# Kernel tuning notes

Measured on AMD Instinct MI355X. Metric: run time of the kernel, lower is better.

Reference implementation:

```python
import jax, jax.numpy as jnp
import numpy as np

B, S, D, H, L = 512, 128, 128, 1024, 128
N_SUB = 4  # fixed dopri5 substeps per observation interval

# Dormand-Prince 5(4) tableau (FSAL form); solution uses 5th-order b weights.
DP_A = (
    (),
    (1/5,),
    (3/40, 9/40),
    (44/45, -56/15, 32/9),
    (19372/6561, -25360/2187, 64448/6561, -212/729),
    (9017/3168, -355/33, 46732/5247, 49/176, -5103/18656),
    (35/384, 0.0, 500/1113, 125/192, -2187/6784, 11/84),
)
DP_B = (35/384, 0.0, 500/1113, 125/192, -2187/6784, 11/84, 0.0)


def _mlp(h, w0, b0, w1, b1, w2, b2):
    # create_mlp(hidden, hidden, hidden, num_layers=3, 'tanh'): Lin-tanh-Lin-tanh-Lin
    h = jnp.tanh(h @ w0.T + b0)
    h = jnp.tanh(h @ w1.T + b1)
    return h @ w2.T + b2


def _gru_cell(x, h, w_ih, w_hh, b_ih, b_hh):
    gi = x @ w_ih.T + b_ih  # [B, 3H]
    gh = h @ w_hh.T + b_hh
    i_r, i_z, i_n = jnp.split(gi, 3, axis=-1)
    h_r, h_z, h_n = jnp.split(gh, 3, axis=-1)
    r = jax.nn.sigmoid(i_r + h_r)
    z = jax.nn.sigmoid(i_z + h_z)
    n = jnp.tanh(i_n + r * h_n)
    return (1.0 - z) * n + z * h


def _dopri5_step(f, h, hs):
    ks = []
    for row in DP_A:
        y = h
        for a, k in zip(row, ks):
            if a != 0.0:
                y = y + (hs * a) * k
        ks.append(f(y))
    out = h
    for b, k in zip(DP_B, ks):
        if b != 0.0:
            out = out + (hs * b) * k
    return out


def _forward(x, t, gru_w_ih, gru_w_hh, gru_b_ih, gru_b_hh,
             w0, b0, w1, b1, w2, b2, mu_w, mu_b, lv_w, lv_b):
    f = lambda h: _mlp(h, w0, b0, w1, b1, w2, b2)  # autonomous ODE func
    bsz = x.shape[0]
    hdim = gru_w_hh.shape[1]
    dts = t[0, 1:, 0] - t[0, :-1, 0]  # [S-1]
    h = _gru_cell(x[:, 0, :], jnp.zeros((bsz, hdim), x.dtype),
                  gru_w_ih, gru_w_hh, gru_b_ih, gru_b_hh)

    def step(h, inp):
        xi, dt = inp
        hs = dt / N_SUB
        for _ in range(N_SUB):
            h = _dopri5_step(f, h, hs)
        h = _gru_cell(xi, h, gru_w_ih, gru_w_hh, gru_b_ih, gru_b_hh)
        return h, None

    h, _ = jax.lax.scan(step, h, (jnp.swapaxes(x[:, 1:, :], 0, 1), dts))
    mu = h @ mu_w.T + mu_b
    logvar = h @ lv_w.T + lv_b
    return mu, logvar


def setup_inputs() -> dict:
    key = jax.random.key(0)
    ks = jax.random.split(key, 12)
    s = 0.02
    return {
        "x": jax.random.normal(ks[0], (B, S, D), jnp.float32),
        "t": jnp.arange(S, dtype=jnp.float32).reshape(1, S, 1) * 0.1,
        "gru_w_ih": jax.random.normal(ks[1], (3 * H, D), jnp.float32) * s,
        "gru_w_hh": jax.random.normal(ks[2], (3 * H, H), jnp.float32) * s,
        "gru_b_ih": jnp.zeros((3 * H,), jnp.float32),
        "gru_b_hh": jnp.zeros((3 * H,), jnp.float32),
        "w0": jax.random.normal(ks[3], (H, H), jnp.float32) * s,
        "b0": jnp.zeros((H,), jnp.float32),
        "w1": jax.random.normal(ks[4], (H, H), jnp.float32) * s,
        "b1": jnp.zeros((H,), jnp.float32),
        "w2": jax.random.normal(ks[5], (H, H), jnp.float32) * s,
        "b2": jnp.zeros((H,), jnp.float32),
        "mu_w": jax.random.normal(ks[6], (L, H), jnp.float32) * s,
        "mu_b": jnp.zeros((L,), jnp.float32),
        "lv_w": jax.random.normal(ks[7], (L, H), jnp.float32) * s,
        "lv_b": jnp.zeros((L,), jnp.float32),
    }


def reference(x, t, gru_w_ih, gru_w_hh, gru_b_ih, gru_b_hh,
              w0, b0, w1, b1, w2, b2, mu_w, mu_b, lv_w, lv_b):
    return _forward(x, t, gru_w_ih, gru_w_hh, gru_b_ih, gru_b_hh,
                    w0, b0, w1, b1, w2, b2, mu_w, mu_b, lv_w, lv_b)
```

## Files before the change

kernel.cpp:

```cpp
#include <hip/hip_runtime.h>
#include <hip/hip_cooperative_groups.h>
#include <math.h>

#define Bz 512
#define Sz 128
#define Dz 128
#define Hz 1024
#define Lz 128
#define NSUB 4

#define GRID 256
#define BLOCK 512
#define NGRP 16
#define GBLK 16

typedef _Float16 half8 __attribute__((ext_vector_type(8)));
typedef float floatx4 __attribute__((ext_vector_type(4)));
typedef unsigned long long u64;

#define MFMA16(a, b, c) __builtin_amdgcn_mfma_f32_16x16x32_f16(a, b, c, 0, 0, 0)

#define ALO_D 4096
#define BHI_O 8192
#define BLO_D 8192
#define CHUNK_HALFS 24576
#define LDS_HALFS 49152

enum { EPI_F32 = 0, EPI_T = 1, EPI_Y = 2, EPI_H = 3 };

__constant__ float DPA_C[6][6] = {
  {0.2f, 0.f, 0.f, 0.f, 0.f, 0.f},
  {0.075f, 0.225f, 0.f, 0.f, 0.f, 0.f},
  {44.f/45.f, -56.f/15.f, 32.f/9.f, 0.f, 0.f, 0.f},
  {19372.f/6561.f, -25360.f/2187.f, 64448.f/6561.f, -212.f/729.f, 0.f, 0.f},
  {9017.f/3168.f, -355.f/33.f, 46732.f/5247.f, 49.f/176.f, -5103.f/18656.f, 0.f},
  {35.f/384.f, 0.f, 500.f/1113.f, 125.f/192.f, -2187.f/6784.f, 11.f/84.f},
};

struct KArgs {
  const float *x, *t, *w_ih, *w_hh, *b_ih, *b_hh;
  const float *w0, *b0, *w1, *b1, *w2, *b2, *mu_w, *mu_b, *lv_w, *lv_b;
  float* out;
  float *h, *gi, *gh;
  unsigned* bar;
  _Float16 *yh, *yl, *t1h, *t1l, *t2h, *t2l, *hhp, *hlp;
  _Float16 *w0h, *w0l, *w1h, *w1l, *w2h, *w2l;
  _Float16 *whhh, *whhl, *wihh, *wihl, *muh, *mulo, *lvh, *lvl;
};

__device__ __forceinline__ float ldc1(const float* p) {
  unsigned v = __hip_atomic_load((unsigned*)p, __ATOMIC_RELAXED, __HIP_MEMORY_SCOPE_AGENT);
  union { unsigned u; float f; } c; c.u = v; return c.f;
}
__device__ __forceinline__ void stc1(float* p, float f) {
  union { float f; unsigned u; } c; c.f = f;
  __hip_atomic_store((unsigned*)p, c.u, __ATOMIC_RELAXED, __HIP_MEMORY_SCOPE_AGENT);
}
__device__ __forceinline__ half8 ldc8h(const _Float16* p) {
  union { u64 u[2]; half8 h; } c;
  c.u[0] = __hip_atomic_load((const u64*)p, __ATOMIC_RELAXED, __HIP_MEMORY_SCOPE_AGENT);
  c.u[1] = __hip_atomic_load(((const u64*)p) + 1, __ATOMIC_RELAXED, __HIP_MEMORY_SCOPE_AGENT);
  return c.h;
}
__device__ __forceinline__ void sth2(_Float16* ph, _Float16* pl, float v) {
  _Float16 h = (_Float16)v;
  _Float16 l = (_Float16)((v - (float)h) * 2048.0f);
  union { _Float16 f; unsigned short u; } ch, cl; ch.f = h; cl.f = l;
  __hip_atomic_store((unsigned short*)ph, ch.u, __ATOMIC_RELAXED, __HIP_MEMORY_SCOPE_AGENT);
  __hip_atomic_store((unsigned short*)pl, cl.u, __ATOMIC_RELAXED, __HIP_MEMORY_SCOPE_AGENT);
}

__device__ __forceinline__ void gbar(unsigned* gb, int jj, unsigned e) {
  asm volatile("s_waitcnt vmcnt(0) lgkmcnt(0)" ::: "memory");
  __syncthreads();
  if (threadIdx.x == 0)
    __hip_atomic_store(&gb[jj], e, __ATOMIC_RELAXED, __HIP_MEMORY_SCOPE_AGENT);
  if (threadIdx.x < 64) {
    const int sl = threadIdx.x & 15;
    while (__hip_atomic_load(&gb[sl], __ATOMIC_RELAXED, __HIP_MEMORY_SCOPE_AGENT) != e)
      __builtin_amdgcn_s_sleep(1);
  }
  __syncthreads();
}

__device__ __forceinline__ void split8(float4 a, float4 b, half8& h, half8& l) {
  float v[8] = {a.x, a.y, a.z, a.w, b.x, b.y, b.z, b.w};
#pragma unroll
  for (int i = 0; i < 8; ++i) {
    _Float16 hh = (_Float16)v[i];
    h[i] = hh;
    l[i] = (_Float16)((v[i] - (float)hh) * 2048.0f);
  }
}

__device__ void convW(const float* __restrict__ W, size_t total,
                      _Float16* __restrict__ hi, _Float16* __restrict__ lo) {
  for (size_t i = (size_t)blockIdx.x * BLOCK + threadIdx.x; i < total;
       i += (size_t)GRID * BLOCK) {
    const float v = W[i];
    const _Float16 h = (_Float16)v;
    hi[i] = h;
    lo[i] = (_Float16)((v - (float)h) * 2048.0f);
  }
}

template<int K, int AM>
__device__ __forceinline__ void mfma_tile(
    const float* __restrict__ Af,
    const _Float16* __restrict__ Ahi, const _Float16* __restrict__ Alo, int lda,
    const _Float16* __restrict__ Whi, const _Float16* __restrict__ Wlo,
    const float* __restrict__ bias,
    float* __restrict__ Cf, _Float16* __restrict__ Chi, _Float16* __restrict__ Clo,
    int ldc, int act, int epi, int stage, float hs,
    const float* __restrict__ hbuf,
    floatx4& K0, floatx4& K1, floatx4& K2, floatx4& K3, floatx4& K4,
    floatx4& Hc,
    int row0, int col0, _Float16* __restrict__ lds)
{
  constexpr int NC = K >> 7;
  const int tid = threadIdx.x;
  const int ln  = tid & 63;
  const int l16 = ln & 15;
  const int qd  = ln >> 4;
  const int wv  = tid >> 6;
  const int wr  = wv >> 2;
  const int wc  = wv & 3;

  const int an   = tid >> 4;
  const int an15 = an & 15, ang = an >> 4;
  const int seg  = tid & 15;
  const int c_ = seg >> 2, q_ = seg & 3;
  const int ua = q_ * 16 + (an15 ^ ((q_ << 1) | (c_ & 1)));
  const int aoff  = (((c_ * 2 + ang) * 64 + ua) << 3);
  const int boff0 = BHI_O + (((c_ * 4 + ang) * 64 + ua) << 3);
  const int boff1 = BHI_O + (((c_ * 4 + 2 + ang) * 64 + ua) << 3);

  const float*    gA  = Af  + (size_t)(row0 + an) * lda + (seg << 3);
  const _Float16* gAh = Ahi + (size_t)(row0 + an) * lda + (seg << 3);
  const _Float16* gAl = Alo + (size_t)(row0 + an) * lda + (seg << 3);
  const _Float16* gW0h = Whi + (size_t)(col0 + an) * K + (seg << 3);
  const _Float16* gW0l = Wlo + (size_t)(col0 + an) * K + (seg << 3);
  const _Float16* gW1h = Whi + (size_t)(col0 + 32 + an) * K + (seg << 3);
  const _Float16* gW1l = Wlo + (size_t)(col0 + 32 + an) * K + (seg << 3);

  floatx4 Phh = {0,0,0,0}, Phl = {0,0,0,0}, Plh = {0,0,0,0}, Pll = {0,0,0,0};

  half8 rah, ral, rw0h, rw0l, rw1h, rw1l;
  float4 ra0, ra1;
  auto load6 = [&](int kk) {
    if (AM == 0) {
      rah = ldc8h(gAh + kk);
      ral = ldc8h(gAl + kk);
    } else {
      ra0 = *(const float4*)(gA + kk);
      ra1 = *(const float4*)(gA + kk + 4);
    }
    rw0h = *(const half8*)(gW0h + kk); rw0l = *(const half8*)(gW0l + kk);
    rw1h = *(const half8*)(gW1h + kk); rw1l = *(const half8*)(gW1l + kk);
  };
  auto store6 = [&](int bufo) {
    if (AM == 1) { half8 h, l; split8(ra0, ra1, h, l); rah = h; ral = l; }
    *(half8*)&lds[bufo + aoff]  = rah;
    *(half8*)&lds[bufo + aoff + ALO_D]  = ral;
    *(half8*)&lds[bufo + boff0] = rw0h;
    *(half8*)&lds[bufo + boff0 + BLO_D] = rw0l;
    *(half8*)&lds[bufo + boff1] = rw1h;
    *(half8*)&lds[bufo + boff1 + BLO_D] = rw1l;
  };

  load6(0);
  __syncthreads();
  store6(0);
  if (NC > 1) load6(128);

#pragma unroll
  for (int c = 0; c < NC; ++c) {
    __syncthreads();
    if (c + 1 < NC) {
      store6(((c + 1) & 1) ? CHUNK_HALFS : 0);
      if (c + 2 < NC) load6((c + 2) << 7);
    }
    const _Float16* __restrict__ lr = lds + ((c & 1) ? CHUNK_HALFS : 0);
#pragma unroll
    for (int kq = 0; kq < 4; ++kq) {
      const int lnw = ln ^ ((qd << 1) | (kq & 1));
      const int ab = ((kq * 2 + wr) * 64 + lnw) << 3;
      const int bb = BHI_O + (((kq * 4 + wc) * 64 + lnw) << 3);
      half8 ah = *(const half8*)&lr[ab];
      half8 al = *(const half8*)&lr[ab + ALO_D];
      half8 bh = *(const half8*)&lr[bb];
      half8 bl = *(const half8*)&lr[bb + BLO_D];
      Phh = MFMA16(ah, bh, Phh);
      Phl = MFMA16(ah, bl, Phl);
      Plh = MFMA16(al, bh, Plh);
      Pll = MFMA16(al, bl, Pll);
    }
  }

  const int col   = col0 + (wc << 4) + l16;
  const int rbase = row0 + (wr << 4) + (qd << 2);
  const float bb = bias[col];
#pragma unroll
  for (int i = 0; i < 4; ++i) {
    float v = Phh[i] + (Phl[i] + Plh[i]) * (1.0f/2048.0f)
            + Pll[i] * (1.0f/4194304.0f) + bb;
    if (act) v = tanhf(v);
    const size_t off = (size_t)(rbase + i) * ldc + col;
    if (epi == EPI_F32) {
      stc1(&Cf[off], v);
    } else if (epi == EPI_T) {
      sth2(Chi + off, Clo + off, v);
    } else {
      if (stage == 0) Hc[i] = ldc1(&hbuf[off]);
      float yv = Hc[i];
      const float* DP = DPA_C[stage];
      if (stage > 0) yv = fmaf(hs * DP[0], K0[i], yv);
      if (stage > 1) { float c1 = DP[1]; if (c1 != 0.f) yv = fmaf(hs * c1, K1[i], yv); }
      if (stage > 2) yv = fmaf(hs * DP[2], K2[i], yv);
      if (stage > 3) yv = fmaf(hs * DP[3], K3[i], yv);
      if (stage > 4) yv = fmaf(hs * DP[4], K4[i], yv);
      yv = fmaf(hs * DP[stage], v, yv);
      if      (stage == 0) K0[i] = v;
      else if (stage == 1) K1[i] = v;
      else if (stage == 2) K2[i] = v;
      else if (stage == 3) K3[i] = v;
      else if (stage == 4) K4[i] = v;
      if (epi == EPI_H) stc1(&Cf[off], yv);
      sth2(Chi + off, Clo + off, yv);
    }
  }
}

template<int K, int AM>
__device__ __forceinline__ void run_phase(
    const float* Af, const _Float16* Ahi, const _Float16* Alo, int lda,
    const _Float16* Whi, const _Float16* Wlo, const float* bias, int N,
    float* Cf, _Float16* Chi, _Float16* Clo, int ldc,
    int act, int epi, int stage, float hs, const float* hbuf,
    floatx4& K0, floatx4& K1, floatx4& K2, floatx4& K3, floatx4& K4,
    floatx4& Hc, int g, int jj, _Float16* lds)
{
  const int tilesN = N >> 6;
  const int row0 = g << 5;
  if (tilesN >= GBLK) {
    const int tn0 = ((jj & 7) << 1) | (jj >> 3);
    for (int i = 0; i < (tilesN >> 4); ++i)
      mfma_tile<K, AM>(Af, Ahi, Alo, lda, Whi, Wlo, bias, Cf, Chi, Clo, ldc,
                       act, epi, stage, hs, hbuf, K0, K1, K2, K3, K4, Hc,
                       row0, (tn0 + (i << 4)) << 6, lds);
  } else {
    if (jj < tilesN)
      mfma_tile<K, AM>(Af, Ahi, Alo, lda, Whi, Wlo, bias, Cf, Chi, Clo, ldc,
                       act, epi, stage, hs, hbuf, K0, K1, K2, K3, K4, Hc,
                       row0, jj << 6, lds);
  }
}

__global__ __launch_bounds__(BLOCK, 2) void ode_gru_kernel(KArgs a) {
  __shared__ __align__(16) _Float16 lds[LDS_HALFS];
  const int g  = blockIdx.x >> 4;
  const int jj = blockIdx.x & 15;
  unsigned* gb = a.bar + (g << 6);
  unsigned ep = 0;

  for (int i = jj * BLOCK + threadIdx.x; i < 32 * Hz; i += GBLK * BLOCK) {
    const size_t o = (size_t)g * 32 * Hz + i;
    stc1(a.h + o, 0.f);
    sth2(a.hhp + o, a.hlp + o, 0.f);
  }

  const size_t E1 = (size_t)Hz * Hz, Ehh = 3 * E1;
  const size_t Eih = (size_t)3 * Hz * Dz, Emu = (size_t)Lz * Hz;
  convW(a.w0,   E1,  a.w0h,  a.w0l);
  convW(a.w1,   E1,  a.w1h,  a.w1l);
  convW(a.w2,   E1,  a.w2h,  a.w2l);
  convW(a.w_hh, Ehh, a.whhh, a.whhl);
  convW(a.w_ih, Eih, a.wihh, a.wihl);
  convW(a.mu_w, Emu, a.muh,  a.mulo);
  convW(a.lv_w, Emu, a.lvh,  a.lvl);
  cooperative_groups::this_grid().sync();

  floatx4 K0 = {0,0,0,0}, K1 = {0,0,0,0}, K2 = {0,0,0,0};
  floatx4 K3 = {0,0,0,0}, K4 = {0,0,0,0}, Hc = {0,0,0,0};

  for (int s = 0; s < Sz; ++s) {
    if (s > 0) {
      const float dt = a.t[s] - a.t[s - 1];
      const float hs = dt * (1.0f / NSUB);
      for (int sub = 0; sub < NSUB; ++sub) {
        for (int st = 0; st < 6; ++st) {
          const _Float16* ah = (st == 0) ? a.hhp : a.yh;
          const _Float16* al = (st == 0) ? a.hlp : a.yl;
          run_phase<Hz, 0>(nullptr, ah, al, Hz, a.w0h, a.w0l, a.b0, Hz,
                           nullptr, a.t1h, a.t1l, Hz, 1, EPI_T, 0, 0.f, nullptr,
                           K0, K1, K2, K3, K4, Hc, g, jj, lds);
          gbar(gb, jj, ++ep);
          run_phase<Hz, 0>(nullptr, a.t1h, a.t1l, Hz, a.w1h, a.w1l, a.b1, Hz,
                           nullptr, a.t2h, a.t2l, Hz, 1, EPI_T, 0, 0.f, nullptr,
                           K0, K1, K2, K3, K4, Hc, g, jj, lds);
          gbar(gb, jj, ++ep);
          if (st < 5) {
            run_phase<Hz, 0>(nullptr, a.t2h, a.t2l, Hz, a.w2h, a.w2l, a.b2, Hz,
                             nullptr, a.yh, a.yl, Hz, 0, EPI_Y, st, hs, a.h,
                             K0, K1, K2, K3, K4, Hc, g, jj, lds);
          } else {
            run_phase<Hz, 0>(nullptr, a.t2h, a.t2l, Hz, a.w2h, a.w2l, a.b2, Hz,
                             a.h, a.hhp, a.hlp, Hz, 0, EPI_H, 5, hs, a.h,
                             K0, K1, K2, K3, K4, Hc, g, jj, lds);
          }
          gbar(gb, jj, ++ep);
        }
      }
    }

    run_phase<Dz, 1>(a.x + (size_t)s * Dz, nullptr, nullptr, Sz * Dz,
                     a.wihh, a.wihl, a.b_ih, 3 * Hz,
                     a.gi, nullptr, nullptr, 3 * Hz, 0, EPI_F32, 0, 0.f, nullptr,
                     K0, K1, K2, K3, K4, Hc, g, jj, lds);
    run_phase<Hz, 0>(nullptr, a.hhp, a.hlp, Hz, a.whhh, a.whhl, a.b_hh, 3 * Hz,
                     a.gh, nullptr, nullptr, 3 * Hz, 0, EPI_F32, 0, 0.f, nullptr,
                     K0, K1, K2, K3, K4, Hc, g, jj, lds);
    gbar(gb, jj, ++ep);

    for (int i = jj * BLOCK + threadIdx.x; i < 32 * Hz; i += GBLK * BLOCK) {
      const int r = g * 32 + (i >> 10);
      const int c = i & (Hz - 1);
      const size_t gx = (size_t)r * 3 * Hz + c;
      const size_t hx = (size_t)r * Hz + c;
      const float ir  = ldc1(a.gi + gx);
      const float iz  = ldc1(a.gi + gx + Hz);
      const float inn = ldc1(a.gi + gx + 2 * Hz);
      const float hr  = ldc1(a.gh + gx);
      const float hzv = ldc1(a.gh + gx + Hz);
      const float hnn = ldc1(a.gh + gx + 2 * Hz);
      const float hv  = ldc1(a.h + hx);
      const float rr  = 1.f / (1.f + expf(-(ir + hr)));
      const float zz  = 1.f / (1.f + expf(-(iz + hzv)));
      const float nnv = tanhf(inn + rr * hnn);
      const float hn  = (1.f - zz) * nnv + zz * hv;
      stc1(a.h + hx, hn);
      sth2(a.hhp + hx, a.hlp + hx, hn);
    }
    gbar(gb, jj, ++ep);
  }

  run_phase<Hz, 0>(nullptr, a.hhp, a.hlp, Hz, a.muh, a.mulo, a.mu_b, Lz,
                   a.out, nullptr, nullptr, Lz, 0, EPI_F32, 0, 0.f, nullptr,
                   K0, K1, K2, K3, K4, Hc, g, jj, lds);
  run_phase<Hz, 0>(nullptr, a.hhp, a.hlp, Hz, a.lvh, a.lvl, a.lv_b, Lz,
                   a.out + (size_t)Bz * Lz, nullptr, nullptr, Lz,
                   0, EPI_F32, 0, 0.f, nullptr,
                   K0, K1, K2, K3, K4, Hc, g, jj, lds);
}

extern "C" void kernel_launch(void* const* d_in, const int* in_sizes, int n_in,
                              void* d_out, int out_size, void* d_ws, size_t ws_size,
                              hipStream_t stream) {
  KArgs a;
  a.x    = (const float*)d_in[0];
  a.t    = (const float*)d_in[1];
  a.w_ih = (const float*)d_in[2];
  a.w_hh = (const float*)d_in[3];
  a.b_ih = (const float*)d_in[4];
  a.b_hh = (const float*)d_in[5];
  a.w0   = (const float*)d_in[6];
  a.b0   = (const float*)d_in[7];
  a.w1   = (const float*)d_in[8];
  a.b1   = (const float*)d_in[9];
  a.w2   = (const float*)d_in[10];
  a.b2   = (const float*)d_in[11];
  a.mu_w = (const float*)d_in[12];
  a.mu_b = (const float*)d_in[13];
  a.lv_w = (const float*)d_in[14];
  a.lv_b = (const float*)d_in[15];
  a.out  = (float*)d_out;

  float* ws = (float*)d_ws;
  const size_t BH = (size_t)Bz * Hz;
  a.h  = ws;
  a.gi = ws + BH;
  a.gh = ws + 4 * BH;
  a.bar = (unsigned*)(ws + 7 * BH);

  _Float16* hv = (_Float16*)(ws + 7 * BH + 1024);
  a.yh  = hv; hv += BH;  a.yl  = hv; hv += BH;
  a.t1h = hv; hv += BH;  a.t1l = hv; hv += BH;
  a.t2h = hv; hv += BH;  a.t2l = hv; hv += BH;
  a.hhp = hv; hv += BH;  a.hlp = hv; hv += BH;
  const size_t E1 = (size_t)Hz * Hz, Ehh = 3 * E1;
  const size_t Eih = (size_t)3 * Hz * Dz, Emu = (size_t)Lz * Hz;
  a.w0h = hv; hv += E1;  a.w0l = hv; hv += E1;
  a.w1h = hv; hv += E1;  a.w1l = hv; hv += E1;
  a.w2h = hv; hv += E1;  a.w2l = hv; hv += E1;
  a.whhh = hv; hv += Ehh; a.whhl = hv; hv += Ehh;
  a.wihh = hv; hv += Eih; a.wihl = hv; hv += Eih;
  a.muh = hv; hv += Emu; a.mulo = hv; hv += Emu;
  a.lvh = hv; hv += Emu; a.lvl = hv; hv += Emu;
  (void)ws_size; (void)in_sizes; (void)n_in; (void)out_size;

  KArgs args_val = a;
  void* params[] = { &args_val };
  hipLaunchCooperativeKernel((void*)ode_gru_kernel, dim3(GRID), dim3(BLOCK),
                             params, 0, stream);
}
```

Baseline: 87.76 ms.

## Switch tile GEMM to 32x32 MFMA with split-K across waves and LDS reduction

New measurement: 126.3 ms. 1.44x slower.

```diff
diff --git a/kernel.cpp b/kernel.cpp
--- a/kernel.cpp
+++ b/kernel.cpp
@@ -16,15 +16,14 @@
 
 typedef _Float16 half8 __attribute__((ext_vector_type(8)));
 typedef float floatx4 __attribute__((ext_vector_type(4)));
+typedef float floatx16 __attribute__((ext_vector_type(16)));
 typedef unsigned long long u64;
 
-#define MFMA16(a, b, c) __builtin_amdgcn_mfma_f32_16x16x32_f16(a, b, c, 0, 0, 0)
-
-#define ALO_D 4096
-#define BHI_O 8192
-#define BLO_D 8192
+#define MFMA32(a, b, c) __builtin_amdgcn_mfma_f32_32x32x16_f16(a, b, c, 0, 0, 0)
+
 #define CHUNK_HALFS 24576
 #define LDS_HALFS 49152
+#define PR 36
 
 enum { EPI_F32 = 0, EPI_T = 1, EPI_Y = 2, EPI_H = 3 };
 
@@ -123,17 +122,18 @@
   const int l16 = ln & 15;
   const int qd  = ln >> 4;
   const int wv  = tid >> 6;
-  const int wr  = wv >> 2;
+  const int wr  = (wv >> 2) & 1;
   const int wc  = wv & 3;
-
-  const int an   = tid >> 4;
-  const int an15 = an & 15, ang = an >> 4;
-  const int seg  = tid & 15;
-  const int c_ = seg >> 2, q_ = seg & 3;
-  const int ua = q_ * 16 + (an15 ^ ((q_ << 1) | (c_ & 1)));
-  const int aoff  = (((c_ * 2 + ang) * 64 + ua) << 3);
-  const int boff0 = BHI_O + (((c_ * 4 + ang) * 64 + ua) << 3);
-  const int boff1 = BHI_O + (((c_ * 4 + 2 + ang) * 64 + ua) << 3);
+  const int pos = wv & 1;
+  const int ks  = wv >> 1;
+
+  const int an  = tid >> 4;
+  const int seg = tid & 15;
+  const int stw = seg >> 1, bw = seg & 1;
+  const int usw = (an + (bw << 5)) ^ (((stw & 3) << 1) | bw);
+  const int aoff  = (stw * 64 + usw) << 3;
+  const int boff0 = 8192 + aoff;
+  const int boff1 = 12288 + aoff;
 
   const float*    gA  = Af  + (size_t)(row0 + an) * lda + (seg << 3);
   const _Float16* gAh = Ahi + (size_t)(row0 + an) * lda + (seg << 3);
@@ -143,7 +143,10 @@
   const _Float16* gW1h = Whi + (size_t)(col0 + 32 + an) * K + (seg << 3);
   const _Float16* gW1l = Wlo + (size_t)(col0 + 32 + an) * K + (seg << 3);
 
-  floatx4 Phh = {0,0,0,0}, Phl = {0,0,0,0}, Plh = {0,0,0,0}, Pll = {0,0,0,0};
+  floatx16 Phh = {0,0,0,0,0,0,0,0,0,0,0,0,0,0,0,0};
+  floatx16 Phl = {0,0,0,0,0,0,0,0,0,0,0,0,0,0,0,0};
+  floatx16 Plh = {0,0,0,0,0,0,0,0,0,0,0,0,0,0,0,0};
+  floatx16 Pll = {0,0,0,0,0,0,0,0,0,0,0,0,0,0,0,0};
 
   half8 rah, ral, rw0h, rw0l, rw1h, rw1l;
   float4 ra0, ra1;
@@ -160,12 +163,12 @@
   };
   auto store6 = [&](int bufo) {
     if (AM == 1) { half8 h, l; split8(ra0, ra1, h, l); rah = h; ral = l; }
-    *(half8*)&lds[bufo + aoff]  = rah;
-    *(half8*)&lds[bufo + aoff + ALO_D]  = ral;
-    *(half8*)&lds[bufo + boff0] = rw0h;
-    *(half8*)&lds[bufo + boff0 + BLO_D] = rw0l;
-    *(half8*)&lds[bufo + boff1] = rw1h;
-    *(half8*)&lds[bufo + boff1 + BLO_D] = rw1l;
+    *(half8*)&lds[bufo + aoff]          = rah;
+    *(half8*)&lds[bufo + aoff + 4096]   = ral;
+    *(half8*)&lds[bufo + boff0]         = rw0h;
+    *(half8*)&lds[bufo + boff0 + 8192]  = rw0l;
+    *(half8*)&lds[bufo + boff1]         = rw1h;
+    *(half8*)&lds[bufo + boff1 + 8192]  = rw1l;
   };
 
   load6(0);
@@ -180,30 +183,58 @@
       store6(((c + 1) & 1) ? CHUNK_HALFS : 0);
       if (c + 2 < NC) load6((c + 2) << 7);
     }
-    const _Float16* __restrict__ lr = lds + ((c & 1) ? CHUNK_HALFS : 0);
+    if ((c & 3) == ks) {
+      const _Float16* __restrict__ lr = lds + ((c & 1) ? CHUNK_HALFS : 0);
 #pragma unroll
-    for (int kq = 0; kq < 4; ++kq) {
-      const int lnw = ln ^ ((qd << 1) | (kq & 1));
-      const int ab = ((kq * 2 + wr) * 64 + lnw) << 3;
-      const int bb = BHI_O + (((kq * 4 + wc) * 64 + lnw) << 3);
-      half8 ah = *(const half8*)&lr[ab];
-      half8 al = *(const half8*)&lr[ab + ALO_D];
-      half8 bh = *(const half8*)&lr[bb];
-      half8 bl = *(const half8*)&lr[bb + BLO_D];
-      Phh = MFMA16(ah, bh, Phh);
-      Phl = MFMA16(ah, bl, Phl);
-      Plh = MFMA16(al, bh, Plh);
-      Pll = MFMA16(al, bl, Pll);
-    }
-  }
+      for (int st = 0; st < 8; ++st) {
+        const int usr = ln ^ (((st & 3) << 1) | (ln >> 5));
+        const int o = (st * 64 + usr) << 3;
+        half8 ah = *(const half8*)&lr[o];
+        half8 al = *(const half8*)&lr[o + 4096];
+        half8 bh = *(const half8*)&lr[8192 + pos * 4096 + o];
+        half8 bl = *(const half8*)&lr[16384 + pos * 4096 + o];
+        Phh = MFMA32(ah, bh, Phh);
+        Phl = MFMA32(ah, bl, Phl);
+        Plh = MFMA32(al, bh, Plh);
+        Pll = MFMA32(al, bl, Pll);
+      }
+    }
+  }
+
+  __syncthreads();
+  float* pf = (float*)lds;
+  {
+    const int c32w = ln & 31, b5 = ln >> 5;
+#pragma unroll
+    for (int jg = 0; jg < 4; ++jg) {
+      const int rb = 8 * jg + 4 * b5;
+      float4 v;
+      v.x = Phh[jg*4+0] + (Phl[jg*4+0] + Plh[jg*4+0]) * (1.0f/2048.0f)
+          + Pll[jg*4+0] * (1.0f/4194304.0f);
+      v.y = Phh[jg*4+1] + (Phl[jg*4+1] + Plh[jg*4+1]) * (1.0f/2048.0f)
+          + Pll[jg*4+1] * (1.0f/4194304.0f);
+      v.z = Phh[jg*4+2] + (Phl[jg*4+2] + Plh[jg*4+2]) * (1.0f/2048.0f)
+          + Pll[jg*4+2] * (1.0f/4194304.0f);
+      v.w = Phh[jg*4+3] + (Phl[jg*4+3] + Plh[jg*4+3]) * (1.0f/2048.0f)
+          + Pll[jg*4+3] * (1.0f/4194304.0f);
+      *(float4*)&pf[(wv * 32 + c32w) * PR + rb] = v;
+    }
+  }
+  __syncthreads();
 
   const int col   = col0 + (wc << 4) + l16;
   const int rbase = row0 + (wr << 4) + (qd << 2);
+  const int pos_e = wc >> 1;
+  const int c32e  = ((wc & 1) << 4) + l16;
+  const int re    = (wr << 4) + (qd << 2);
+  floatx4 p0 = *(const floatx4*)&pf[((0 + pos_e) * 32 + c32e) * PR + re];
+  floatx4 p1 = *(const floatx4*)&pf[((2 + pos_e) * 32 + c32e) * PR + re];
+  floatx4 p2 = *(const floatx4*)&pf[((4 + pos_e) * 32 + c32e) * PR + re];
+  floatx4 p3 = *(const floatx4*)&pf[((6 + pos_e) * 32 + c32e) * PR + re];
   const float bb = bias[col];
 #pragma unroll
   for (int i = 0; i < 4; ++i) {
-    float v = Phh[i] + (Phl[i] + Plh[i]) * (1.0f/2048.0f)
-            + Pll[i] * (1.0f/4194304.0f) + bb;
+    float v = p0[i] + p1[i] + p2[i] + p3[i] + bb;
     if (act) v = tanhf(v);
     const size_t off = (size_t)(rbase + i) * ldc + col;
     if (epi == EPI_F32) {
```

## Split K chunks across wave halves with LDS cross-wave reduction in MFMA tile

Applied to the files above, without the earlier changes.

Result: slower. 108.6 ms (+23.8%).

```diff
diff --git a/kernel.cpp b/kernel.cpp
--- a/kernel.cpp
+++ b/kernel.cpp
@@ -123,8 +123,10 @@
   const int l16 = ln & 15;
   const int qd  = ln >> 4;
   const int wv  = tid >> 6;
-  const int wr  = wv >> 2;
+  const int wr  = (wv >> 2) & 1;
   const int wc  = wv & 3;
+  const int pos = wv & 3;
+  const int ks  = wv >> 2;
 
   const int an   = tid >> 4;
   const int an15 = an & 15, ang = an >> 4;
@@ -143,7 +145,11 @@
   const _Float16* gW1h = Whi + (size_t)(col0 + 32 + an) * K + (seg << 3);
   const _Float16* gW1l = Wlo + (size_t)(col0 + 32 + an) * K + (seg << 3);
 
-  floatx4 Phh = {0,0,0,0}, Phl = {0,0,0,0}, Plh = {0,0,0,0}, Pll = {0,0,0,0};
+  floatx4 acc[2][4];
+#pragma unroll
+  for (int f = 0; f < 2; ++f)
+#pragma unroll
+    for (int p = 0; p < 4; ++p) acc[f][p] = (floatx4){0, 0, 0, 0};
 
   half8 rah, ral, rw0h, rw0l, rw1h, rw1l;
   float4 ra0, ra1;
@@ -160,11 +166,11 @@
   };
   auto store6 = [&](int bufo) {
     if (AM == 1) { half8 h, l; split8(ra0, ra1, h, l); rah = h; ral = l; }
-    *(half8*)&lds[bufo + aoff]  = rah;
+    *(half8*)&lds[bufo + aoff]          = rah;
     *(half8*)&lds[bufo + aoff + ALO_D]  = ral;
-    *(half8*)&lds[bufo + boff0] = rw0h;
+    *(half8*)&lds[bufo + boff0]         = rw0h;
     *(half8*)&lds[bufo + boff0 + BLO_D] = rw0l;
-    *(half8*)&lds[bufo + boff1] = rw1h;
+    *(half8*)&lds[bufo + boff1]         = rw1h;
     *(half8*)&lds[bufo + boff1 + BLO_D] = rw1l;
   };
 
@@ -180,30 +186,53 @@
       store6(((c + 1) & 1) ? CHUNK_HALFS : 0);
       if (c + 2 < NC) load6((c + 2) << 7);
     }
-    const _Float16* __restrict__ lr = lds + ((c & 1) ? CHUNK_HALFS : 0);
-#pragma unroll
-    for (int kq = 0; kq < 4; ++kq) {
-      const int lnw = ln ^ ((qd << 1) | (kq & 1));
-      const int ab = ((kq * 2 + wr) * 64 + lnw) << 3;
-      const int bb = BHI_O + (((kq * 4 + wc) * 64 + lnw) << 3);
-      half8 ah = *(const half8*)&lr[ab];
-      half8 al = *(const half8*)&lr[ab + ALO_D];
-      half8 bh = *(const half8*)&lr[bb];
-      half8 bl = *(const half8*)&lr[bb + BLO_D];
-      Phh = MFMA16(ah, bh, Phh);
-      Phl = MFMA16(ah, bl, Phl);
-      Plh = MFMA16(al, bh, Plh);
-      Pll = MFMA16(al, bl, Pll);
-    }
-  }
+    if ((c & 1) == ks) {
+      const _Float16* __restrict__ lr = lds + ((c & 1) ? CHUNK_HALFS : 0);
+#pragma unroll
+      for (int kq = 0; kq < 4; ++kq) {
+        const int lnw = ln ^ ((qd << 1) | (kq & 1));
+        const int bb = BHI_O + (((kq * 4 + pos) * 64 + lnw) << 3);
+        half8 bh = *(const half8*)&lr[bb];
+        half8 bl = *(const half8*)&lr[bb + BLO_D];
+#pragma unroll
+        for (int f = 0; f < 2; ++f) {
+          const int ab = ((kq * 2 + f) * 64 + lnw) << 3;
+          half8 ah = *(const half8*)&lr[ab];
+          half8 al = *(const half8*)&lr[ab + ALO_D];
+          acc[f][0] = MFMA16(ah, bh, acc[f][0]);
+          acc[f][1] = MFMA16(ah, bl, acc[f][1]);
+          acc[f][2] = MFMA16(al, bh, acc[f][2]);
+          acc[f][3] = MFMA16(al, bl, acc[f][3]);
+        }
+      }
+    }
+  }
+
+  __syncthreads();
+  float* pf = (float*)lds;
+#pragma unroll
+  for (int f = 0; f < 2; ++f) {
+    float4 v;
+    v.x = acc[f][0][0] + (acc[f][1][0] + acc[f][2][0]) * (1.0f/2048.0f)
+        + acc[f][3][0] * (1.0f/4194304.0f);
+    v.y = acc[f][0][1] + (acc[f][1][1] + acc[f][2][1]) * (1.0f/2048.0f)
+        + acc[f][3][1] * (1.0f/4194304.0f);
+    v.z = acc[f][0][2] + (acc[f][1][2] + acc[f][2][2]) * (1.0f/2048.0f)
+        + acc[f][3][2] * (1.0f/4194304.0f);
+    v.w = acc[f][0][3] + (acc[f][1][3] + acc[f][2][3]) * (1.0f/2048.0f)
+        + acc[f][3][3] * (1.0f/4194304.0f);
+    *(float4*)&pf[((((ks << 2) | pos) * 2 + f) * 64 + ln) << 2] = v;
+  }
+  __syncthreads();
 
   const int col   = col0 + (wc << 4) + l16;
   const int rbase = row0 + (wr << 4) + (qd << 2);
+  floatx4 p0 = *(const floatx4*)&pf[(((wc) * 2 + wr) * 64 + ln) << 2];
+  floatx4 p1 = *(const floatx4*)&pf[(((4 + wc) * 2 + wr) * 64 + ln) << 2];
   const float bb = bias[col];
 #pragma unroll
   for (int i = 0; i < 4; ++i) {
-    float v = Phh[i] + (Phl[i] + Plh[i]) * (1.0f/2048.0f)
-            + Pll[i] * (1.0f/4194304.0f) + bb;
+    float v = p0[i] + p1[i] + bb;
     if (act) v = tanhf(v);
     const size_t off = (size_t)(rbase + i) * ldc + col;
     if (epi == EPI_F32) {
```
